# Optimization experiments

Hardware: AMD Instinct MI355X
Metric: run time of the kernel (lower is better)

## Reference

```python
import jax, jax.numpy as jnp
import numpy as np

N_USER = 50000
N_ITEM = 50000
E = 800000
C_IN = 128
C_OUT = 128
N_HEADS = 4


def setup_inputs() -> dict:
    key = jax.random.key(0)
    ks = jax.random.split(key, 12)
    xav = lambda k, shp: jax.random.uniform(k, shp, jnp.float32, -1.0, 1.0) * jnp.sqrt(6.0 / (shp[0] + shp[1]))
    return {
        'x_user': jax.random.normal(ks[0], (N_USER, C_IN), jnp.float32),
        'x_item': jax.random.normal(ks[1], (N_ITEM, C_IN), jnp.float32),
        'ei_u2i': jnp.stack([jax.random.randint(ks[2], (E,), 0, N_USER, jnp.int32),
                             jax.random.randint(ks[3], (E,), 0, N_ITEM, jnp.int32)]),
        'ei_i2u': jnp.stack([jax.random.randint(ks[4], (E,), 0, N_ITEM, jnp.int32),
                             jax.random.randint(ks[5], (E,), 0, N_USER, jnp.int32)]),
        'W_nb': xav(ks[6], (C_OUT, C_IN)),
        'b_nb': jnp.zeros((C_OUT,), jnp.float32),
        'W_self': xav(ks[7], (C_OUT, C_IN)),
        'b_self': jnp.zeros((C_OUT,), jnp.float32),
        'in_proj_w': xav(ks[8], (3 * C_OUT, C_OUT)),
        'in_proj_b': jnp.zeros((3 * C_OUT,), jnp.float32),
        'out_proj_w': xav(ks[9], (C_OUT, C_OUT)),
        'out_proj_b': jnp.zeros((C_OUT,), jnp.float32),
    }


def _multi_aggr(h_src, edge_index, n_dst):
    """h_src: already lin_neighbor-transformed src features [N_src, C].
    Returns [n_dst, 4, C] stacked as [max, min, sum, mean] (torch_scatter semantics:
    empty segments -> 0; mean divides by clamp(count, 1))."""
    src, dst = edge_index[0], edge_index[1]
    msgs = h_src[src]  # [E, C]  (linear commutes with gather)
    s = jax.ops.segment_sum(msgs, dst, num_segments=n_dst)
    cnt = jax.ops.segment_sum(jnp.ones((msgs.shape[0],), msgs.dtype), dst, num_segments=n_dst)
    has = (cnt > 0)[:, None]
    mean = s / jnp.maximum(cnt, 1.0)[:, None]
    mx = jnp.where(has, jax.ops.segment_max(msgs, dst, num_segments=n_dst), 0.0)
    mn = jnp.where(has, jax.ops.segment_min(msgs, dst, num_segments=n_dst), 0.0)
    return jnp.stack([mx, mn, s, mean], axis=1)  # [n_dst, 4, C]


def _mha(tokens, in_proj_w, in_proj_b, out_proj_w, out_proj_b):
    """torch nn.MultiheadAttention (eval mode, batch_first=False). tokens: [S, N, C]."""
    S, N, C = tokens.shape
    H, Dh = N_HEADS, C // N_HEADS
    qkv = tokens @ in_proj_w.T + in_proj_b            # [S, N, 3C]
    q, k, v = jnp.split(qkv, 3, axis=-1)
    q = q.reshape(S, N, H, Dh) * (1.0 / jnp.sqrt(jnp.asarray(Dh, tokens.dtype)))
    k = k.reshape(S, N, H, Dh)
    v = v.reshape(S, N, H, Dh)
    scores = jnp.einsum('snhd,tnhd->nhst', q, k)       # [N, H, S, S]
    attn = jax.nn.softmax(scores, axis=-1)
    o = jnp.einsum('nhst,tnhd->snhd', attn, v).reshape(S, N, C)
    return o @ out_proj_w.T + out_proj_b               # [S, N, C]


def reference(x_user, x_item, ei_u2i, ei_i2u, W_nb, b_nb, W_self, b_self,
              in_proj_w, in_proj_b, out_proj_w, out_proj_b):
    # shared neighbor linear applied once per node type, then gathered per edge
    h_user = x_user @ W_nb.T + b_nb
    h_item = x_item @ W_nb.T + b_nb
    aggr_item = _multi_aggr(h_user, ei_u2i, N_ITEM)    # user->item : [N_item, 4, C]
    aggr_user = _multi_aggr(h_item, ei_i2u, N_USER)    # item->user : [N_user, 4, C]

    def per_type(x, aggr):
        self_feat = x @ W_self.T + b_self              # [N, C]
        # tokens: [self, max, min, sum, mean] -> [5, N, C]
        tokens = jnp.concatenate([self_feat[None], jnp.transpose(aggr, (1, 0, 2))], axis=0)
        attn_out = _mha(tokens, in_proj_w, in_proj_b, out_proj_w, out_proj_b)
        return self_feat + attn_out.mean(axis=0)

    out_user = per_type(x_user, aggr_user)
    out_item = per_type(x_item, aggr_item)
    return (out_user, out_item)
```

## Files before the change

### kernel.cpp

```cpp
#include <hip/hip_runtime.h>
#include <hip/hip_bf16.h>


#define C 128
#define NHEAD 4
#define DH 32
#define QK_SCALE 0.17677669529663687f

typedef __attribute__((ext_vector_type(8))) short bf16x8;
typedef __attribute__((ext_vector_type(4))) short short4v;
typedef __attribute__((ext_vector_type(2))) short short2v;
typedef __attribute__((ext_vector_type(4))) float f32x4;

__device__ __forceinline__ short f2bf(float f) {
    unsigned u = __float_as_uint(f);
    unsigned r = u + 0x7FFFu + ((u >> 16) & 1u);
    return (short)(r >> 16);
}

__global__ __launch_bounds__(256) void prep_kernel(
    const float* __restrict__ Wip, unsigned* __restrict__ img,
    const float* __restrict__ Wnb, const float* __restrict__ Wself,
    unsigned* __restrict__ imgW,
    int* __restrict__ curA, int nA, int* __restrict__ curB, int nB)
{
    const int tid = threadIdx.x;
    const int bid = (int)blockIdx.x;
    if (bid < 96) {
        int id = bid * 256 + tid;
        int ks = id / (384 * 16);
        int rem = id - ks * (384 * 16);
        int n = rem >> 4, kk = rem & 15;
        float a = Wip[(size_t)n * C + ks * 32 + kk * 2 + 0];
        float b = Wip[(size_t)n * C + ks * 32 + kk * 2 + 1];
        unsigned pa = ((unsigned)(unsigned short)f2bf(a))
                    | (((unsigned)(unsigned short)f2bf(b)) << 16);
        img[(size_t)ks * 6144 + n * 16 + kk] = pa;
    } else if (bid < 160) {
        int id = (bid - 96) * 256 + tid;
        int ks = id / (256 * 16);
        int rem = id - ks * (256 * 16);
        int n = rem >> 4, kk = rem & 15;
        const float* src = (n < 128) ? &Wnb[(size_t)n * C]
                                     : &Wself[(size_t)(n - 128) * C];
        float a = src[ks * 32 + kk * 2 + 0];
        float b = src[ks * 32 + kk * 2 + 1];
        unsigned pa = ((unsigned)(unsigned short)f2bf(a))
                    | (((unsigned)(unsigned short)f2bf(b)) << 16);
        imgW[(size_t)ks * 4096 + n * 16 + kk] = pa;
    } else {
        int i = (bid - 160) * 256 + tid;
        if (i < nA) curA[i] = 0;
        else if (i < nA + nB) curB[i - nA] = 0;
    }
}

__global__ __launch_bounds__(256, 4) void transform_kernel(
    const float* __restrict__ xu, const float* __restrict__ xi,
    int NU, int NTOT,
    const unsigned short* __restrict__ wnsbf,
    const float* __restrict__ bnb, const float* __restrict__ bself,
    unsigned short* __restrict__ h_bf, unsigned short* __restrict__ self_bf,
    float* __restrict__ selfout)
{
    __shared__ char Ash[64 * 272];
    __shared__ float biasS[256];

    const int tid = threadIdx.x;
    const int lane = tid & 63;
    const int wv = tid >> 6;
    const int row0 = blockIdx.x * 64;

    biasS[tid] = (tid < 128) ? bnb[tid] : bself[tid - 128];

#pragma unroll
    for (int i = 0; i < 8; i++) {
        int id = tid + i * 256;
        int r = id >> 5, c4 = id & 31;
        int row = row0 + r;
        float4 v = make_float4(0.f, 0.f, 0.f, 0.f);
        if (row < NTOT) {
            v = (row < NU) ? ((const float4*)xu)[(size_t)row * 32 + c4]
                           : ((const float4*)xi)[(size_t)(row - NU) * 32 + c4];
        }
        short4v b;
        b.x = f2bf(v.x); b.y = f2bf(v.y); b.z = f2bf(v.z); b.w = f2bf(v.w);
        *(short4v*)(Ash + r * 272 + c4 * 8) = b;
    }
    __syncthreads();

    const int quad = lane >> 4;
    const int col16 = lane & 15;

    f32x4 acc[4][4];
#pragma unroll
    for (int mt = 0; mt < 4; mt++)
#pragma unroll
        for (int nt = 0; nt < 4; nt++) acc[mt][nt] = (f32x4){0.f, 0.f, 0.f, 0.f};

#pragma unroll
    for (int ks = 0; ks < 4; ks++) {
        bf16x8 bfv[4];
#pragma unroll
        for (int nt = 0; nt < 4; nt++) {
            int n = (wv * 4 + nt) * 16 + col16;
            bfv[nt] = *(const bf16x8*)((const char*)wnsbf
                        + (size_t)ks * 16384 + (size_t)n * 64 + quad * 16);
        }
#pragma unroll
        for (int mt = 0; mt < 4; mt++) {
            bf16x8 af = *(const bf16x8*)(Ash + (mt * 16 + col16) * 272
                                         + ks * 64 + quad * 16);
#pragma unroll
            for (int nt = 0; nt < 4; nt++)
                acc[mt][nt] = __builtin_amdgcn_mfma_f32_16x16x32_bf16(
                                  af, bfv[nt], acc[mt][nt], 0, 0, 0);
        }
    }

#pragma unroll
    for (int mt = 0; mt < 4; mt++) {
#pragma unroll
        for (int reg = 0; reg < 4; reg++) {
            int row = row0 + mt * 16 + quad * 4 + reg;
            if (row < NTOT) {
#pragma unroll
                for (int nt = 0; nt < 4; nt++) {
                    int col = (wv * 4 + nt) * 16 + col16;
                    float v = acc[mt][nt][reg] + biasS[col];
                    if (wv < 2) {
                        h_bf[(size_t)row * C + col] = (unsigned short)f2bf(v);
                    } else {
                        selfout[(size_t)row * C + (col - 128)] = v;
                        self_bf[(size_t)row * C + (col - 128)] = (unsigned short)f2bf(v);
                    }
                }
            }
        }
    }
}

__global__ __launch_bounds__(256) void hist2_kernel(
    const int* __restrict__ dstA, int nA, int* __restrict__ curA,
    const int* __restrict__ dstB, int nB, int* __restrict__ curB)
{
    int i = blockIdx.x * 256 + threadIdx.x;
    if (i < nA) atomicAdd(&curA[dstA[i]], 1);
    else if (i < nA + nB) atomicAdd(&curB[dstB[i - nA]], 1);
}

__global__ __launch_bounds__(1024) void scan2_kernel(
    int* __restrict__ curA, int nA, int* __restrict__ curB, int nB)
{
    int* cur = (blockIdx.x == 0) ? curA : curB;
    const int n = (blockIdx.x == 0) ? nA : nB;

    __shared__ int wsum[16];
    __shared__ int carryS;
    const int tid = threadIdx.x, lane = tid & 63, wv = tid >> 6;
    if (tid == 0) carryS = 0;
    __syncthreads();
    for (int base = 0; base < n; base += 4096) {
        int i0 = base + tid * 4;
        int v0 = 0, v1 = 0, v2 = 0, v3 = 0;
        if (i0 + 3 < n) {
            int4 t = *(const int4*)&cur[i0];
            v0 = t.x; v1 = t.y; v2 = t.z; v3 = t.w;
        } else {
            if (i0 < n) v0 = cur[i0];
            if (i0 + 1 < n) v1 = cur[i0 + 1];
            if (i0 + 2 < n) v2 = cur[i0 + 2];
            if (i0 + 3 < n) v3 = cur[i0 + 3];
        }
        int s1 = v0 + v1, s2 = s1 + v2, s3 = s2 + v3;
        int x = s3;
#pragma unroll
        for (int d = 1; d < 64; d <<= 1) {
            int t = __shfl_up(x, d, 64);
            if (lane >= d) x += t;
        }
        if (lane == 63) wsum[wv] = x;
        int carry = carryS;
        __syncthreads();
        int wpre = 0;
#pragma unroll
        for (int w2 = 0; w2 < 16; w2++) wpre += (w2 < wv) ? wsum[w2] : 0;
        int excl = x - s3 + wpre + carry;
        if (i0 + 3 < n) {
            int4 st; st.x = excl; st.y = excl + v0; st.z = excl + s1; st.w = excl + s2;
            *(int4*)&cur[i0] = st;
        } else {
            if (i0 < n) cur[i0] = excl;
            if (i0 + 1 < n) cur[i0 + 1] = excl + v0;
            if (i0 + 2 < n) cur[i0 + 2] = excl + s1;
            if (i0 + 3 < n) cur[i0 + 3] = excl + s2;
        }
        __syncthreads();
        if (tid == 0) {
            int t = 0;
#pragma unroll
            for (int w2 = 0; w2 < 16; w2++) t += wsum[w2];
            carryS = carry + t;
        }
        __syncthreads();
    }
}

__global__ __launch_bounds__(256) void fill2_kernel(
    const int* __restrict__ srcA, const int* __restrict__ dstA, int nA,
    int* __restrict__ curA, unsigned short* __restrict__ csrA,
    const int* __restrict__ srcB, const int* __restrict__ dstB, int nB,
    int* __restrict__ curB, unsigned short* __restrict__ csrB)
{
    int i = blockIdx.x * 256 + threadIdx.x;
    if (i < nA) {
        int p = atomicAdd(&curA[dstA[i]], 1);
        csrA[p] = (unsigned short)srcA[i];
    } else if (i < nA + nB) {
        int j = i - nA;
        int p = atomicAdd(&curB[dstB[j]], 1);
        csrB[p] = (unsigned short)srcB[j];
    }
}

#define ATN 4

__global__ __launch_bounds__(256, 8) void attn_fused_kernel(
    const unsigned short* __restrict__ h_bf, const unsigned short* __restrict__ csr,
    const int* __restrict__ cur, const unsigned short* __restrict__ self_bf,
    const short* __restrict__ wipbf, const float* __restrict__ bip,
    float* __restrict__ omean_g, int n_nodes)
{
    __shared__ char Ash[16 * 272];
    __shared__ float cinv[ATN];

    const int tid = threadIdx.x;
    const int lane = tid & 63;
    const int wv = tid >> 6;
    const int node0 = blockIdx.x * ATN;

    if (tid < 128) {
        int r = tid >> 5, c4 = tid & 31;
        int node = node0 + r;
        short4v b = {0, 0, 0, 0};
        if (node < n_nodes)
            b = *(const short4v*)(self_bf + (size_t)node * C + c4 * 4);
        *(short4v*)(Ash + (r * 4) * 272 + c4 * 8) = b;
    }

    {
        const unsigned* h2 = (const unsigned*)h_bf;
        int node = node0 + wv;
        float2 vs = make_float2(0.f, 0.f);
        float2 vmx = make_float2(-3.4e38f, -3.4e38f);
        float2 vmn = make_float2(3.4e38f, 3.4e38f);
        int deg = 0;
        if (node < n_nodes) {
            int start = (node == 0) ? 0 : cur[node - 1];
            int end = cur[node];
            deg = end - start;
            int e = start;
            for (; e + 8 <= end; e += 8) {
                unsigned v[8];
#pragma unroll
                for (int i = 0; i < 8; i++) {
                    int s = csr[e + i];
                    v[i] = h2[(size_t)s * 64 + lane];
                }
#pragma unroll
                for (int i = 0; i < 8; i++) {
                    float fx = __uint_as_float(v[i] << 16);
                    float fy = __uint_as_float(v[i] & 0xFFFF0000u);
                    vs.x += fx; vs.y += fy;
                    vmx.x = fmaxf(vmx.x, fx); vmx.y = fmaxf(vmx.y, fy);
                    vmn.x = fminf(vmn.x, fx); vmn.y = fminf(vmn.y, fy);
                }
            }
            if (e < end) {
                int last = end - 1;
                unsigned v[8];
#pragma unroll
                for (int i = 0; i < 8; i++) {
                    int idx = e + i;
                    int s = csr[(idx <= last) ? idx : last];
                    v[i] = h2[(size_t)s * 64 + lane];
                }
#pragma unroll
                for (int i = 0; i < 8; i++) {
                    if (e + i <= last) {
                        float fx = __uint_as_float(v[i] << 16);
                        float fy = __uint_as_float(v[i] & 0xFFFF0000u);
                        vs.x += fx; vs.y += fy;
                        vmx.x = fmaxf(vmx.x, fx); vmx.y = fmaxf(vmx.y, fy);
                        vmn.x = fminf(vmn.x, fx); vmn.y = fminf(vmn.y, fy);
                    }
                }
            }
        }
        if (deg == 0) {
            vmx = make_float2(0.f, 0.f);
            vmn = make_float2(0.f, 0.f);
        }
        short2v p;
        p.x = f2bf(vmx.x); p.y = f2bf(vmx.y);
        *(short2v*)(Ash + (wv * 4 + 1) * 272 + lane * 4) = p;
        p.x = f2bf(vmn.x); p.y = f2bf(vmn.y);
        *(short2v*)(Ash + (wv * 4 + 2) * 272 + lane * 4) = p;
        p.x = f2bf(vs.x); p.y = f2bf(vs.y);
        *(short2v*)(Ash + (wv * 4 + 3) * 272 + lane * 4) = p;
        if (lane == 0) cinv[wv] = 1.f / (float)max(deg, 1);
    }
    __syncthreads();

    const int quad = lane >> 4;
    const int col16 = lane & 15;

    f32x4 acc[6];
#pragma unroll
    for (int t = 0; t < 6; t++) acc[t] = (f32x4){0.f, 0.f, 0.f, 0.f};

#pragma unroll
    for (int ks = 0; ks < 4; ks++) {
        bf16x8 af = *(const bf16x8*)(Ash + col16 * 272 + ks * 64 + quad * 16);
#pragma unroll
        for (int t = 0; t < 6; t++) {
            int nb = wv * 32 + (t & 1) * 16 + (t >> 1) * 128 + col16;
            bf16x8 bfr = *(const bf16x8*)((const char*)wipbf
                          + (size_t)ks * 24576 + (size_t)nb * 64 + quad * 16);
            acc[t] = __builtin_amdgcn_mfma_f32_16x16x32_bf16(af, bfr, acc[t], 0, 0, 0);
        }
    }

    const float ci = cinv[quad];
    const float cis = ci * QK_SCALE;

    const float bq0 = bip[wv * 32 + col16];
    const float bq1 = bip[wv * 32 + 16 + col16];
    const float bk0 = bip[128 + wv * 32 + col16];
    const float bk1 = bip[128 + wv * 32 + 16 + col16];
    const float bv0 = bip[256 + wv * 32 + col16];
    const float bv1 = bip[256 + wv * 32 + 16 + col16];
    const float bq0s = bq0 * QK_SCALE;
    const float bq1s = bq1 * QK_SCALE;

    float k0[5], k1[5];
#pragma unroll
    for (int s = 0; s < 4; s++) { k0[s] = acc[2][s] + bk0; k1[s] = acc[3][s] + bk1; }
    k0[4] = fmaf(acc[2][3], ci, bk0);
    k1[4] = fmaf(acc[3][3], ci, bk1);

    float wj[5] = {0.f, 0.f, 0.f, 0.f, 0.f};
#pragma unroll
    for (int i = 0; i < 5; i++) {
        float qi0 = (i < 4) ? fmaf(acc[0][i], QK_SCALE, bq0s)
                            : fmaf(acc[0][3], cis, bq0s);
        float qi1 = (i < 4) ? fmaf(acc[1][i], QK_SCALE, bq1s)
                            : fmaf(acc[1][3], cis, bq1s);
        float sv[5];
#pragma unroll
        for (int j = 0; j < 5; j++) sv[j] = qi0 * k0[j] + qi1 * k1[j];
#pragma unroll
        for (int j = 0; j < 5; j++) {
            sv[j] += __shfl_xor(sv[j], 1, 16);
            sv[j] += __shfl_xor(sv[j], 2, 16);
            sv[j] += __shfl_xor(sv[j], 4, 16);
            sv[j] += __shfl_xor(sv[j], 8, 16);
        }
        float m = sv[0];
#pragma unroll
        for (int j = 1; j < 5; j++) m = fmaxf(m, sv[j]);
        float e[5], l = 0.f;
#pragma unroll
        for (int j = 0; j < 5; j++) { e[j] = __expf(sv[j] - m); l += e[j]; }
        float inv = 0.2f / l;
#pragma unroll
        for (int j = 0; j < 5; j++) wj[j] = fmaf(e[j], inv, wj[j]);
    }

    float o0 = 0.f, o1 = 0.f;
#pragma unroll
    for (int j = 0; j < 5; j++) {
        float v0 = (j < 4) ? (acc[4][j] + bv0) : fmaf(acc[4][3], ci, bv0);
        float v1 = (j < 4) ? (acc[5][j] + bv1) : fmaf(acc[5][3], ci, bv1);
        o0 = fmaf(wj[j], v0, o0);
        o1 = fmaf(wj[j], v1, o1);
    }

    int node = node0 + quad;
    if (node < n_nodes) {
        omean_g[(size_t)node * C + wv * 32 + col16] = o0;
        omean_g[(size_t)node * C + wv * 32 + 16 + col16] = o1;
    }
}

__global__ __launch_bounds__(256, 3) void outproj_kernel(
    const float* __restrict__ omean_g, const float* __restrict__ Wop,
    const float* __restrict__ bop, float* __restrict__ out, int M)
{
    __shared__ float As[64 * 132];
    __shared__ float Bs[128 * 36];
    __shared__ float bopS[C];

    const int tid = threadIdx.x;
    const int m0 = blockIdx.x * 64;

    if (tid < C) bopS[tid] = bop[tid];

#pragma unroll
    for (int i = 0; i < 8; i++) {
        int id = tid + i * 256;
        int r = id >> 5, c4 = id & 31;
        float4 v = make_float4(0.f, 0.f, 0.f, 0.f);
        if (m0 + r < M) v = ((const float4*)omean_g)[(size_t)(m0 + r) * 32 + c4];
        *(float4*)&As[r * 132 + c4 * 4] = v;
    }

    const int tn = tid & 31;
    const int tm = tid >> 5;
    float acc[8][4];
#pragma unroll
    for (int m = 0; m < 8; m++)
#pragma unroll
        for (int j = 0; j < 4; j++) acc[m][j] = 0.f;

    for (int ks = 0; ks < 4; ks++) {
        __syncthreads();
#pragma unroll
        for (int i = 0; i < 4; i++) {
            int id = tid + i * 256;
            int n = id >> 3, q = id & 7;
            float4 w = ((const float4*)Wop)[(size_t)n * 32 + ks * 8 + q];
            *(float4*)&Bs[n * 36 + q * 4] = w;
        }
        __syncthreads();

        for (int k4 = 0; k4 < 8; k4++) {
            float4 a[8];
#pragma unroll
            for (int m = 0; m < 8; m++)
                a[m] = *(const float4*)&As[(tm * 8 + m) * 132 + ks * 32 + k4 * 4];
            float4 b[4];
#pragma unroll
            for (int j = 0; j < 4; j++)
                b[j] = *(const float4*)&Bs[(tn + 32 * j) * 36 + k4 * 4];
#pragma unroll
            for (int m = 0; m < 8; m++) {
                float4 av = a[m];
#pragma unroll
                for (int j = 0; j < 4; j++) {
                    float4 bv = b[j];
                    acc[m][j] += av.x * bv.x + av.y * bv.y
                               + av.z * bv.z + av.w * bv.w;
                }
            }
        }
    }

#pragma unroll
    for (int m = 0; m < 8; m++) {
        int row = m0 + tm * 8 + m;
        if (row < M) {
#pragma unroll
            for (int j = 0; j < 4; j++) {
                int col = tn + 32 * j;
                float* o = &out[(size_t)row * C + col];
                *o += acc[m][j] + bopS[col];
            }
        }
    }
}

extern "C" void kernel_launch(void* const* d_in, const int* in_sizes, int n_in,
                              void* d_out, int out_size, void* d_ws, size_t ws_size,
                              hipStream_t stream) {
    const float* x_user = (const float*)d_in[0];
    const float* x_item = (const float*)d_in[1];
    const int*   ei_u2i = (const int*)d_in[2];
    const int*   ei_i2u = (const int*)d_in[3];
    const float* W_nb   = (const float*)d_in[4];
    const float* b_nb   = (const float*)d_in[5];
    const float* W_self = (const float*)d_in[6];
    const float* b_self = (const float*)d_in[7];
    const float* Wip    = (const float*)d_in[8];
    const float* bip    = (const float*)d_in[9];
    const float* Wop    = (const float*)d_in[10];
    const float* bop    = (const float*)d_in[11];

    const int NU = in_sizes[0] / C;
    const int NI = in_sizes[1] / C;
    const int E1 = in_sizes[2] / 2;
    const int E2 = in_sizes[3] / 2;
    const int NTOT = NU + NI;

    float* ws = (float*)d_ws;
    short* wipbf            = (short*)ws;
    unsigned short* wnsbf   = (unsigned short*)(ws + 24576);
    unsigned short* h_bf    = (unsigned short*)(ws + 24576 + 16384);
    const size_t rc = (size_t)NTOT * C;
    unsigned short* self_bf = h_bf + rc;
    float* omean_all        = (float*)(self_bf + rc);
    int*   curA             = (int*)(omean_all + rc);
    int*   curB             = curA + NI;
    unsigned short* csrA16  = (unsigned short*)(curB + NU);
    unsigned short* csrB16  = csrA16 + E1;

    unsigned short* h_user_bf = h_bf;
    unsigned short* h_item_bf = h_bf + (size_t)NU * C;
    unsigned short* self_user_bf = self_bf;
    unsigned short* self_item_bf = self_bf + (size_t)NU * C;
    float* om_user = omean_all;
    float* om_item = omean_all + (size_t)NU * C;

    prep_kernel<<<160 + (NTOT + 255) / 256, 256, 0, stream>>>(
        Wip, (unsigned*)wipbf, W_nb, W_self, (unsigned*)wnsbf,
        curA, NI, curB, NU);

    transform_kernel<<<(NTOT + 63) / 64, 256, 0, stream>>>(
        x_user, x_item, NU, NTOT, wnsbf, b_nb, b_self,
        h_bf, self_bf, (float*)d_out);

    hist2_kernel<<<(E1 + E2 + 255) / 256, 256, 0, stream>>>(
        ei_u2i + E1, E1, curA, ei_i2u + E2, E2, curB);

    scan2_kernel<<<2, 1024, 0, stream>>>(curA, NI, curB, NU);

    fill2_kernel<<<(E1 + E2 + 255) / 256, 256, 0, stream>>>(
        ei_u2i, ei_u2i + E1, E1, curA, csrA16,
        ei_i2u, ei_i2u + E2, E2, curB, csrB16);

    attn_fused_kernel<<<(NU + ATN - 1) / ATN, 256, 0, stream>>>(
        h_item_bf, csrB16, curB, self_user_bf, wipbf, bip, om_user, NU);

    attn_fused_kernel<<<(NI + ATN - 1) / ATN, 256, 0, stream>>>(
        h_user_bf, csrA16, curA, self_item_bf, wipbf, bip, om_item, NI);

    outproj_kernel<<<(NTOT + 63) / 64, 256, 0, stream>>>(
        omean_all, Wop, bop, (float*)d_out, NTOT);
}
```

Baseline: 603.3 us.

## Overlap histogram and CSR fill with transform and attention kernels

Folds the edge histogram into extra blocks of the transform kernel, so counting runs alongside the node GEMM. Splits the CSR fill: the i2u fill stays standalone, while the u2i fill runs as extra blocks appended to the first attention launch, overlapping with user-side attention. Also widens the scan to 8 elements per thread and processes 4 edges per thread in the hist and fill loops. This removes kernel launches and idle gaps, but adds resource and branch overhead to the fused kernels, and the attention blocks can compete with atomic-heavy blocks.

```diff
diff --git a/kernel.cpp b/kernel.cpp
--- a/kernel.cpp
+++ b/kernel.cpp
@@ -55,18 +55,33 @@
     }
 }
 
-__global__ __launch_bounds__(256, 4) void transform_kernel(
+__global__ __launch_bounds__(256, 4) void transform_hist_kernel(
     const float* __restrict__ xu, const float* __restrict__ xi,
     int NU, int NTOT,
     const unsigned short* __restrict__ wnsbf,
     const float* __restrict__ bnb, const float* __restrict__ bself,
     unsigned short* __restrict__ h_bf, unsigned short* __restrict__ self_bf,
-    float* __restrict__ selfout)
+    float* __restrict__ selfout,
+    const int* __restrict__ dstA, int nEA, int* __restrict__ curA,
+    const int* __restrict__ dstB, int nEB, int* __restrict__ curB, int TB)
 {
+    const int tid = threadIdx.x;
+
+    if ((int)blockIdx.x >= TB) {
+        int gid = ((int)blockIdx.x - TB) * 256 + tid;
+        int base = gid * 4;
+#pragma unroll
+        for (int k = 0; k < 4; k++) {
+            int i = base + k;
+            if (i < nEA) atomicAdd(&curA[dstA[i]], 1);
+            else if (i < nEA + nEB) atomicAdd(&curB[dstB[i - nEA]], 1);
+        }
+        return;
+    }
+
     __shared__ char Ash[64 * 272];
     __shared__ float biasS[256];
 
-    const int tid = threadIdx.x;
     const int lane = tid & 63;
     const int wv = tid >> 6;
     const int row0 = blockIdx.x * 64;
@@ -140,15 +155,6 @@
     }
 }
 
-__global__ __launch_bounds__(256) void hist2_kernel(
-    const int* __restrict__ dstA, int nA, int* __restrict__ curA,
-    const int* __restrict__ dstB, int nB, int* __restrict__ curB)
-{
-    int i = blockIdx.x * 256 + threadIdx.x;
-    if (i < nA) atomicAdd(&curA[dstA[i]], 1);
-    else if (i < nA + nB) atomicAdd(&curB[dstB[i - nA]], 1);
-}
-
 __global__ __launch_bounds__(1024) void scan2_kernel(
     int* __restrict__ curA, int nA, int* __restrict__ curB, int nB)
 {
@@ -160,20 +166,23 @@
     const int tid = threadIdx.x, lane = tid & 63, wv = tid >> 6;
     if (tid == 0) carryS = 0;
     __syncthreads();
-    for (int base = 0; base < n; base += 4096) {
-        int i0 = base + tid * 4;
-        int v0 = 0, v1 = 0, v2 = 0, v3 = 0;
-        if (i0 + 3 < n) {
-            int4 t = *(const int4*)&cur[i0];
-            v0 = t.x; v1 = t.y; v2 = t.z; v3 = t.w;
+    for (int base = 0; base < n; base += 8192) {
+        int i0 = base + tid * 8;
+        int v[8];
+        if (i0 + 7 < n) {
+            int4 a = *(const int4*)&cur[i0];
+            int4 b = *(const int4*)&cur[i0 + 4];
+            v[0] = a.x; v[1] = a.y; v[2] = a.z; v[3] = a.w;
+            v[4] = b.x; v[5] = b.y; v[6] = b.z; v[7] = b.w;
         } else {
-            if (i0 < n) v0 = cur[i0];
-            if (i0 + 1 < n) v1 = cur[i0 + 1];
-            if (i0 + 2 < n) v2 = cur[i0 + 2];
-            if (i0 + 3 < n) v3 = cur[i0 + 3];
-        }
-        int s1 = v0 + v1, s2 = s1 + v2, s3 = s2 + v3;
-        int x = s3;
+#pragma unroll
+            for (int k = 0; k < 8; k++) v[k] = (i0 + k < n) ? cur[i0 + k] : 0;
+        }
+        int s[8];
+        s[0] = v[0];
+#pragma unroll
+        for (int k = 1; k < 8; k++) s[k] = s[k - 1] + v[k];
+        int x = s[7];
 #pragma unroll
         for (int d = 1; d < 64; d <<= 1) {
             int t = __shfl_up(x, d, 64);
@@ -185,15 +194,17 @@
         int wpre = 0;
 #pragma unroll
         for (int w2 = 0; w2 < 16; w2++) wpre += (w2 < wv) ? wsum[w2] : 0;
-        int excl = x - s3 + wpre + carry;
-        if (i0 + 3 < n) {
-            int4 st; st.x = excl; st.y = excl + v0; st.z = excl + s1; st.w = excl + s2;
-            *(int4*)&cur[i0] = st;
+        int excl = x - s[7] + wpre + carry;
+        if (i0 + 7 < n) {
+            int4 a, b;
+            a.x = excl;        a.y = excl + s[0]; a.z = excl + s[1]; a.w = excl + s[2];
+            b.x = excl + s[3]; b.y = excl + s[4]; b.z = excl + s[5]; b.w = excl + s[6];
+            *(int4*)&cur[i0] = a;
+            *(int4*)&cur[i0 + 4] = b;
         } else {
-            if (i0 < n) cur[i0] = excl;
-            if (i0 + 1 < n) cur[i0 + 1] = excl + v0;
-            if (i0 + 2 < n) cur[i0 + 2] = excl + s1;
-            if (i0 + 3 < n) cur[i0 + 3] = excl + s2;
+#pragma unroll
+            for (int k = 0; k < 8; k++)
+                if (i0 + k < n) cur[i0 + k] = excl + (k ? s[k - 1] : 0);
         }
         __syncthreads();
         if (tid == 0) {
@@ -206,20 +217,18 @@
     }
 }
 
-__global__ __launch_bounds__(256) void fill2_kernel(
-    const int* __restrict__ srcA, const int* __restrict__ dstA, int nA,
-    int* __restrict__ curA, unsigned short* __restrict__ csrA,
-    const int* __restrict__ srcB, const int* __restrict__ dstB, int nB,
-    int* __restrict__ curB, unsigned short* __restrict__ csrB)
+__global__ __launch_bounds__(256) void fill_kernel(
+    const int* __restrict__ src, const int* __restrict__ dst, int nE,
+    int* __restrict__ cur, unsigned short* __restrict__ csr)
 {
-    int i = blockIdx.x * 256 + threadIdx.x;
-    if (i < nA) {
-        int p = atomicAdd(&curA[dstA[i]], 1);
-        csrA[p] = (unsigned short)srcA[i];
-    } else if (i < nA + nB) {
-        int j = i - nA;
-        int p = atomicAdd(&curB[dstB[j]], 1);
-        csrB[p] = (unsigned short)srcB[j];
+    int base = (blockIdx.x * 256 + threadIdx.x) * 4;
+#pragma unroll
+    for (int k = 0; k < 4; k++) {
+        int i = base + k;
+        if (i < nE) {
+            int p = atomicAdd(&cur[dst[i]], 1);
+            csr[p] = (unsigned short)src[i];
+        }
     }
 }
 
@@ -229,12 +238,28 @@
     const unsigned short* __restrict__ h_bf, const unsigned short* __restrict__ csr,
     const int* __restrict__ cur, const unsigned short* __restrict__ self_bf,
     const short* __restrict__ wipbf, const float* __restrict__ bip,
-    float* __restrict__ omean_g, int n_nodes)
+    float* __restrict__ omean_g, int n_nodes, int nAttnBlocks,
+    const int* __restrict__ srcF, const int* __restrict__ dstF, int nEF,
+    int* __restrict__ curF, unsigned short* __restrict__ csrF)
 {
     __shared__ char Ash[16 * 272];
     __shared__ float cinv[ATN];
 
     const int tid = threadIdx.x;
+
+    if ((int)blockIdx.x >= nAttnBlocks) {
+        int base = (((int)blockIdx.x - nAttnBlocks) * 256 + tid) * 4;
+#pragma unroll
+        for (int k = 0; k < 4; k++) {
+            int i = base + k;
+            if (i < nEF) {
+                int p = atomicAdd(&curF[dstF[i]], 1);
+                csrF[p] = (unsigned short)srcF[i];
+            }
+        }
+        return;
+    }
+
     const int lane = tid & 63;
     const int wv = tid >> 6;
     const int node0 = blockIdx.x * ATN;
@@ -515,24 +540,29 @@
         Wip, (unsigned*)wipbf, W_nb, W_self, (unsigned*)wnsbf,
         curA, NI, curB, NU);
 
-    transform_kernel<<<(NTOT + 63) / 64, 256, 0, stream>>>(
+    const int TB = (NTOT + 63) / 64;
+    const int HB = (E1 + E2 + 1023) / 1024;
+    transform_hist_kernel<<<TB + HB, 256, 0, stream>>>(
         x_user, x_item, NU, NTOT, wnsbf, b_nb, b_self,
-        h_bf, self_bf, (float*)d_out);
-
-    hist2_kernel<<<(E1 + E2 + 255) / 256, 256, 0, stream>>>(
-        ei_u2i + E1, E1, curA, ei_i2u + E2, E2, curB);
+        h_bf, self_bf, (float*)d_out,
+        ei_u2i + E1, E1, curA, ei_i2u + E2, E2, curB, TB);
 
     scan2_kernel<<<2, 1024, 0, stream>>>(curA, NI, curB, NU);
 
-    fill2_kernel<<<(E1 + E2 + 255) / 256, 256, 0, stream>>>(
-        ei_u2i, ei_u2i + E1, E1, curA, csrA16,
+    fill_kernel<<<(E2 + 1023) / 1024, 256, 0, stream>>>(
         ei_i2u, ei_i2u + E2, E2, curB, csrB16);
 
-    attn_fused_kernel<<<(NU + ATN - 1) / ATN, 256, 0, stream>>>(
-        h_item_bf, csrB16, curB, self_user_bf, wipbf, bip, om_user, NU);
-
-    attn_fused_kernel<<<(NI + ATN - 1) / ATN, 256, 0, stream>>>(
-        h_user_bf, csrA16, curA, self_item_bf, wipbf, bip, om_item, NI);
+    const int nbB = (NU + ATN - 1) / ATN;
+    const int FBA = (E1 + 1023) / 1024;
+    attn_fused_kernel<<<nbB + FBA, 256, 0, stream>>>(
+        h_item_bf, csrB16, curB, self_user_bf, wipbf, bip, om_user, NU, nbB,
+        ei_u2i, ei_u2i + E1, E1, curA, csrA16);
+
+    const int nbA = (NI + ATN - 1) / ATN;
+    attn_fused_kernel<<<nbA, 256, 0, stream>>>(
+        h_user_bf, csrA16, curA, self_item_bf, wipbf, bip, om_item, NI, nbA,
+        (const int*)nullptr, (const int*)nullptr, 0,
+        (int*)nullptr, (unsigned short*)nullptr);
 
     outproj_kernel<<<(NTOT + 63) / 64, 256, 0, stream>>>(
         omean_all, Wop, bop, (float*)d_out, NTOT);
```

Result: faster. 579.9 us (-3.9%).
